# Kernel optimization log

Measured on AMD Instinct MI355X. Metric: run time of the kernel, lower is better.

Reference implementation:

```python
import jax, jax.numpy as jnp
import numpy as np

L, C, F, H, W = 4, 512, 2048, 8, 4   # layers, channels, filter, heads, window
HD = C // H                          # head_dim = 64
B, T = 4, 1024
EPS = 1e-6


def setup_inputs() -> dict:
    key = jax.random.key(0)
    ks = jax.random.split(key, 12)
    def n(k, shape, s=0.02):
        return jax.random.normal(k, shape, dtype=jnp.float32) * s
    return {
        "x": jax.random.normal(ks[0], (B, C, T), dtype=jnp.float32),
        "mask": jnp.ones((B, 1, T), dtype=jnp.float32),
        "qw": n(ks[1], (L, C, C)), "qb": jnp.zeros((L, C), jnp.float32),
        "kw": n(ks[2], (L, C, C)), "kb": jnp.zeros((L, C), jnp.float32),
        "vw": n(ks[3], (L, C, C)), "vb": jnp.zeros((L, C), jnp.float32),
        "ow": n(ks[4], (L, C, C)), "ob": jnp.zeros((L, C), jnp.float32),
        "emb_rel_k": n(ks[5], (L, 2 * W + 1, HD), 0.01),
        "emb_rel_v": n(ks[6], (L, 2 * W + 1, HD), 0.01),
        "ln1_g": jnp.ones((L, C), jnp.float32), "ln1_b": jnp.zeros((L, C), jnp.float32),
        "w1": n(ks[7], (L, F, C)), "b1": jnp.zeros((L, F), jnp.float32),
        "w2": n(ks[8], (L, C, F)), "b2": jnp.zeros((L, C), jnp.float32),
        "ln2_g": jnp.ones((L, C), jnp.float32), "ln2_b": jnp.zeros((L, C), jnp.float32),
    }


def _conv1(x, w, b):
    # 1x1 Conv1d: (B,Cin,T) x (Cout,Cin) -> (B,Cout,T)
    return jnp.einsum('oc,bct->bot', w, x) + b[None, :, None]


def _ln(x, g, b):
    # LayerNorm over channel dim of (B,C,T)
    m = jnp.mean(x, axis=1, keepdims=True)
    v = jnp.var(x, axis=1, keepdims=True)
    return (x - m) * jax.lax.rsqrt(v + EPS) * g[None, :, None] + b[None, :, None]


def reference(x, mask, qw, qb, kw, kb, vw, vb, ow, ob, emb_rel_k, emb_rel_v,
              ln1_g, ln1_b, w1, b1, w2, b2, ln2_g, ln2_b):
    Bv, Cv, Tv = x.shape
    pos = jnp.arange(Tv)
    rel = pos[None, :] - pos[:, None]           # (T,T) j - i
    outside = jnp.abs(rel) > W
    idx = jnp.clip(rel, -W, W) + W              # (T,T) in [0, 2W]
    am = mask[:, :, None, :]                    # (B,1,1,T)
    inv_scale = 1.0 / jnp.sqrt(jnp.float32(HD))
    for i in range(L):
        res = x
        q = _conv1(x, qw[i], qb[i]).reshape(Bv, H, HD, Tv).transpose(0, 1, 3, 2) * inv_scale
        k = _conv1(x, kw[i], kb[i]).reshape(Bv, H, HD, Tv).transpose(0, 1, 3, 2)
        v = _conv1(x, vw[i], vb[i]).reshape(Bv, H, HD, Tv).transpose(0, 1, 3, 2)
        rk = jnp.where(outside[:, :, None], 0.0, emb_rel_k[i][idx])  # (T,T,HD)
        rv = jnp.where(outside[:, :, None], 0.0, emb_rel_v[i][idx])
        scores = jnp.einsum('bhid,bhjd->bhij', q, k) + jnp.einsum('bhid,ijd->bhij', q, rk)
        scores = jnp.where(am == 0, -jnp.inf, scores)
        attn = jax.nn.softmax(scores, axis=-1)
        o = jnp.einsum('bhij,bhjd->bhid', attn, v) + jnp.einsum('bhij,ijd->bhid', attn, rv)
        o = o.transpose(0, 1, 3, 2).reshape(Bv, Cv, Tv)
        x = _ln(res + _conv1(o, ow[i], ob[i]), ln1_g[i], ln1_b[i])
        res = x
        h = jax.nn.relu(_conv1(x * mask, w1[i], b1[i])) * mask
        h = _conv1(h, w2[i], b2[i]) * mask
        x = _ln(res + h, ln2_g[i], ln2_b[i])
        x = x * mask
    return x
```

## Files before the change

kernel.cpp:

```cpp
#include <hip/hip_runtime.h>

#define BQ 4
#define CQ 512
#define TQ 1024
#define FQ 2048
#define LQ 4
#define HQ 8
#define MT (BQ * TQ)

typedef __attribute__((ext_vector_type(8))) short short8;
typedef __attribute__((ext_vector_type(4))) float floatx4;

#define MFMA16(a, b, c) __builtin_amdgcn_mfma_f32_16x16x32_bf16(a, b, c, 0, 0, 0)

static __device__ __forceinline__ unsigned short f2bf(float f) {
  union { float f; unsigned u; } v; v.f = f;
  unsigned r = v.u + 0x7fff + ((v.u >> 16) & 1);
  return (unsigned short)(r >> 16);
}

static __device__ __forceinline__ void async_copy16(const void* g, void* l) {
  __builtin_amdgcn_global_load_lds(
      (const __attribute__((address_space(1))) void*)g,
      (__attribute__((address_space(3))) void*)l, 16, 0, 0);
}

__global__ __launch_bounds__(256) void mfma_gemm(
    const unsigned short* __restrict__ A, const unsigned short* __restrict__ B,
    void* __restrict__ Y, const float* __restrict__ bias,
    const float* __restrict__ mask, int M, int N, int K, int lda, int ldb,
    long long kofs, long long sYb, float scale, int flags)
{
  const int tid = threadIdx.x;
  const int w = tid >> 6, lane = tid & 63;
  const int wm = w >> 1, wn = w & 1;
  const int m0 = blockIdx.y * 128, n0 = blockIdx.x * 128;
  const size_t ko = (size_t)blockIdx.z * kofs;

  __shared__ unsigned short sA[128 * 32];
  __shared__ unsigned short sB[128 * 32];

  floatx4 acc[4][4];
#pragma unroll
  for (int i = 0; i < 4; i++)
#pragma unroll
    for (int j = 0; j < 4; j++) acc[i][j] = floatx4{0.f, 0.f, 0.f, 0.f};

  const int srow = lane >> 2;
  const int skel = (lane & 3) * 8;
  const int col = lane & 15, gq = lane >> 4;

  for (int k0 = 0; k0 < K; k0 += 32) {
#pragma unroll
    for (int r = 0; r < 2; r++) {
      int c = r * 4 + w;
      async_copy16(&A[(size_t)(m0 + c * 16 + srow) * lda + ko + k0 + skel],
                   &sA[c * 512]);
      async_copy16(&B[(size_t)(n0 + c * 16 + srow) * ldb + ko + k0 + skel],
                   &sB[c * 512]);
    }
    __syncthreads();

    short8 af[4], bfr[4];
#pragma unroll
    for (int im = 0; im < 4; im++)
      af[im] = *(const short8*)&sA[(wm * 64 + im * 16 + col) * 32 + gq * 8];
#pragma unroll
    for (int in = 0; in < 4; in++)
      bfr[in] = *(const short8*)&sB[(wn * 64 + in * 16 + col) * 32 + gq * 8];
#pragma unroll
    for (int im = 0; im < 4; im++)
#pragma unroll
      for (int in = 0; in < 4; in++)
        acc[im][in] = MFMA16(af[im], bfr[in], acc[im][in]);
    __syncthreads();
  }

  const bool relu  = flags & 1;
  const bool prem  = flags & 2;
  const bool postm = flags & 4;
  const bool bf16o = flags & 16;
  const bool raw   = flags & 32;
  float* Yf = (float*)Y + (size_t)blockIdx.z * sYb;
  unsigned short* Yh = (unsigned short*)Y;

#pragma unroll
  for (int im = 0; im < 4; im++)
#pragma unroll
    for (int in = 0; in < 4; in++) {
      int nn = n0 + wn * 64 + in * 16 + col;
      float bn = raw ? 0.f : bias[nn];
#pragma unroll
      for (int reg = 0; reg < 4; reg++) {
        int mm = m0 + wm * 64 + im * 16 + gq * 4 + reg;
        float val = acc[im][in][reg];
        if (raw) {
          Yf[(size_t)mm * N + nn] = val;
        } else {
          float mv = (prem || postm) ? mask[mm] : 1.f;
          if (prem) val *= mv;
          val = (val + bn) * scale;
          if (relu) val = fmaxf(val, 0.f);
          if (postm) val *= mv;
          if (bf16o) Yh[(size_t)mm * N + nn] = f2bf(val);
          else       Yf[(size_t)mm * N + nn] = val;
        }
      }
    }
}

__global__ __launch_bounds__(256) void mfma_gemm64(
    const unsigned short* __restrict__ A, const unsigned short* __restrict__ B,
    float* __restrict__ Y, int M, int N, int K, int lda, int ldb,
    long long kofs, long long sYb)
{
  const int tid = threadIdx.x;
  const int w = tid >> 6, lane = tid & 63;
  const int wm = w >> 1, wn = w & 1;
  const int m0 = blockIdx.y * 128, n0 = blockIdx.x * 64;
  const size_t ko = (size_t)blockIdx.z * kofs;

  __shared__ unsigned short sA[128 * 32];
  __shared__ unsigned short sB[64 * 32];

  floatx4 acc[4][2];
#pragma unroll
  for (int i = 0; i < 4; i++)
#pragma unroll
    for (int j = 0; j < 2; j++) acc[i][j] = floatx4{0.f, 0.f, 0.f, 0.f};

  const int srow = lane >> 2;
  const int skel = (lane & 3) * 8;
  const int col = lane & 15, gq = lane >> 4;

  for (int k0 = 0; k0 < K; k0 += 32) {
    async_copy16(&A[(size_t)(m0 + w * 16 + srow) * lda + ko + k0 + skel],
                 &sA[w * 512]);
    async_copy16(&A[(size_t)(m0 + (w + 4) * 16 + srow) * lda + ko + k0 + skel],
                 &sA[(w + 4) * 512]);
    async_copy16(&B[(size_t)(n0 + w * 16 + srow) * ldb + ko + k0 + skel],
                 &sB[w * 512]);
    __syncthreads();

    short8 af[4], bfr[2];
#pragma unroll
    for (int im = 0; im < 4; im++)
      af[im] = *(const short8*)&sA[(wm * 64 + im * 16 + col) * 32 + gq * 8];
#pragma unroll
    for (int in = 0; in < 2; in++)
      bfr[in] = *(const short8*)&sB[(wn * 32 + in * 16 + col) * 32 + gq * 8];
#pragma unroll
    for (int im = 0; im < 4; im++)
#pragma unroll
      for (int in = 0; in < 2; in++)
        acc[im][in] = MFMA16(af[im], bfr[in], acc[im][in]);
    __syncthreads();
  }

  float* Yf = Y + (size_t)blockIdx.z * sYb;
#pragma unroll
  for (int im = 0; im < 4; im++)
#pragma unroll
    for (int in = 0; in < 2; in++) {
      int nn = n0 + wn * 32 + in * 16 + col;
#pragma unroll
      for (int reg = 0; reg < 4; reg++) {
        int mm = m0 + wm * 64 + im * 16 + gq * 4 + reg;
        Yf[(size_t)mm * N + nn] = acc[im][in][reg];
      }
    }
}

__global__ __launch_bounds__(256) void qkv_gemm(
    const unsigned short* __restrict__ A, const unsigned short* __restrict__ B,
    unsigned short* __restrict__ qo, unsigned short* __restrict__ ko2,
    unsigned short* __restrict__ vo, const float* __restrict__ qb,
    const float* __restrict__ kb, const float* __restrict__ vb)
{
  const int tid = threadIdx.x;
  const int w = tid >> 6, lane = tid & 63;
  const int wm = w >> 1, wn = w & 1;
  const int m0 = blockIdx.y * 128, n0 = blockIdx.x * 128;

  __shared__ unsigned short sA[128 * 32];
  __shared__ unsigned short sB[128 * 32];

  floatx4 acc[4][4];
#pragma unroll
  for (int i = 0; i < 4; i++)
#pragma unroll
    for (int j = 0; j < 4; j++) acc[i][j] = floatx4{0.f, 0.f, 0.f, 0.f};

  const int srow = lane >> 2;
  const int skel = (lane & 3) * 8;
  const int col = lane & 15, gq = lane >> 4;

  for (int k0 = 0; k0 < CQ; k0 += 32) {
#pragma unroll
    for (int r = 0; r < 2; r++) {
      int c = r * 4 + w;
      async_copy16(&A[(size_t)(m0 + c * 16 + srow) * CQ + k0 + skel],
                   &sA[c * 512]);
      async_copy16(&B[(size_t)(n0 + c * 16 + srow) * CQ + k0 + skel],
                   &sB[c * 512]);
    }
    __syncthreads();

    short8 af[4], bfr[4];
#pragma unroll
    for (int im = 0; im < 4; im++)
      af[im] = *(const short8*)&sA[(wm * 64 + im * 16 + col) * 32 + gq * 8];
#pragma unroll
    for (int in = 0; in < 4; in++)
      bfr[in] = *(const short8*)&sB[(wn * 64 + in * 16 + col) * 32 + gq * 8];
#pragma unroll
    for (int im = 0; im < 4; im++)
#pragma unroll
      for (int in = 0; in < 4; in++)
        acc[im][in] = MFMA16(af[im], bfr[in], acc[im][in]);
    __syncthreads();
  }

  const int seg = n0 >> 9;
  const int nbase = n0 - seg * 512;

  if (seg < 2) {
    unsigned short* Yh = (seg == 0) ? qo : ko2;
    const float* bp = (seg == 0) ? qb : kb;
    const float scale = (seg == 0) ? 0.125f : 1.f;
#pragma unroll
    for (int im = 0; im < 4; im++)
#pragma unroll
      for (int in = 0; in < 4; in++) {
        int nn = nbase + wn * 64 + in * 16 + col;
        float bn = bp[nn];
#pragma unroll
        for (int reg = 0; reg < 4; reg++) {
          int mm = m0 + wm * 64 + im * 16 + gq * 4 + reg;
          Yh[(size_t)mm * CQ + nn] = f2bf((acc[im][in][reg] + bn) * scale);
        }
      }
  } else {
#pragma unroll
    for (int im = 0; im < 4; im++)
#pragma unroll
      for (int in = 0; in < 4; in++) {
        int nn = nbase + wn * 64 + in * 16 + col;
        float bn = vb[nn];
        int mm0 = m0 + wm * 64 + im * 16 + gq * 4;
        int bz = mm0 >> 10, t = mm0 & 1023;
        ushort4 uv = {f2bf(acc[im][in][0] + bn), f2bf(acc[im][in][1] + bn),
                      f2bf(acc[im][in][2] + bn), f2bf(acc[im][in][3] + bn)};
        *(ushort4*)&vo[((size_t)bz * CQ + nn) * TQ + t] = uv;
      }
  }
}

__global__ __launch_bounds__(256) void attn_kernel(
    const unsigned short* __restrict__ qt, const unsigned short* __restrict__ kt,
    const unsigned short* __restrict__ vt, const float* __restrict__ mask,
    const float* __restrict__ rk, const float* __restrict__ rv,
    unsigned short* __restrict__ o)
{
  const int b = blockIdx.z, h = blockIdx.y;
  const int w = threadIdx.x >> 6;
  const int lane = threadIdx.x & 63;
  const int col = lane & 15, g = lane >> 4;
  const int i0 = blockIdx.x * 64 + w * 16;

  const unsigned short* qb = qt + (size_t)b * TQ * CQ + h * 64;
  const unsigned short* kb = kt + (size_t)b * TQ * CQ + h * 64;
  const unsigned short* vb = vt + ((size_t)b * CQ + h * 64) * TQ;
  unsigned short* ob = o + (size_t)b * TQ * CQ + h * 64;

  __shared__ unsigned short sK[2][64 * 64];
  __shared__ unsigned short sV[2][64 * 64];
  __shared__ unsigned short pbuf[4][16][72];
  __shared__ float rkdl[4][16][9];
  __shared__ float pband[4][16][9];
  __shared__ float smask[TQ];

  short8 qf0 = *(const short8*)&qb[(size_t)(i0 + col) * CQ + g * 8];
  short8 qf1 = *(const short8*)&qb[(size_t)(i0 + col) * CQ + 32 + g * 8];

  {
    short8 rb0 = {0, 0, 0, 0, 0, 0, 0, 0}, rb1 = rb0;
    if (col < 9) {
#pragma unroll
      for (int i = 0; i < 8; i++) {
        rb0[i] = (short)f2bf(rk[col * 64 + g * 8 + i]);
        rb1[i] = (short)f2bf(rk[col * 64 + 32 + g * 8 + i]);
      }
    }
    floatx4 rc = {0.f, 0.f, 0.f, 0.f};
    rc = MFMA16(qf0, rb0, rc);
    rc = MFMA16(qf1, rb1, rc);
    if (col < 9) {
#pragma unroll
      for (int reg = 0; reg < 4; reg++) rkdl[w][g * 4 + reg][col] = rc[reg];
    }
  }
  for (int e = lane; e < 144; e += 64) pband[w][e / 9][e % 9] = 0.f;
  {
    float4 mvv = *(const float4*)&mask[(size_t)b * TQ + threadIdx.x * 4];
    *(float4*)&smask[threadIdx.x * 4] = mvv;
  }

  const int prow = lane >> 3;
  const int pblk = (lane & 7) ^ prow;
  const int eblk0 = ((0 * 4 + g) ^ (col & 7)) * 8;
  const int eblk1 = ((1 * 4 + g) ^ (col & 7)) * 8;

#pragma unroll
  for (int q = 0; q < 2; q++) {
    int s = w * 2 + q;
    async_copy16(&kb[(size_t)(s * 8 + prow) * CQ + pblk * 8], &sK[0][s * 512]);
    async_copy16(&vb[(size_t)(s * 8 + prow) * TQ + 0 + pblk * 8], &sV[0][s * 512]);
  }

  float l_lane[4] = {0.f, 0.f, 0.f, 0.f};
  floatx4 oacc[4];
#pragma unroll
  for (int r = 0; r < 4; r++) oacc[r] = floatx4{0.f, 0.f, 0.f, 0.f};

  for (int jt = 0; jt < 16; jt++) {
    const int cur = jt & 1, nx = cur ^ 1;
    __syncthreads();
    if (jt < 15) {
      const int j0n = (jt + 1) * 64;
#pragma unroll
      for (int q = 0; q < 2; q++) {
        int s = w * 2 + q;
        async_copy16(&kb[(size_t)(j0n + s * 8 + prow) * CQ + pblk * 8],
                     &sK[nx][s * 512]);
        async_copy16(&vb[(size_t)(s * 8 + prow) * TQ + j0n + pblk * 8],
                     &sV[nx][s * 512]);
      }
    }
    const int j0 = jt * 64;

    floatx4 sc[4];
#pragma unroll
    for (int jg = 0; jg < 4; jg++) {
      const int r = (jg * 16 + col) * 64;
      short8 kf0 = *(const short8*)&sK[cur][r + eblk0];
      short8 kf1 = *(const short8*)&sK[cur][r + eblk1];
      floatx4 z = {0.f, 0.f, 0.f, 0.f};
      z = MFMA16(qf0, kf0, z);
      sc[jg] = MFMA16(qf1, kf1, z);
    }

    const bool inband = (j0 <= i0 + 19) && (j0 + 63 >= i0 - 4);

    float p[4][4];
#pragma unroll
    for (int reg = 0; reg < 4; reg++) {
      const int ig = i0 + g * 4 + reg;
#pragma unroll
      for (int jg = 0; jg < 4; jg++) {
        float s = sc[jg][reg];
        if (inband) {
          int dlt = j0 + jg * 16 + col - ig + 4;
          if (dlt >= 0 && dlt < 9) s += rkdl[w][g * 4 + reg][dlt];
        }
        float pv = (smask[j0 + jg * 16 + col] == 0.f) ? 0.f : __expf(s);
        p[reg][jg] = pv;
        l_lane[reg] += pv;
      }
    }

    if (inband) {
#pragma unroll
      for (int reg = 0; reg < 4; reg++) {
        const int row = g * 4 + reg;
#pragma unroll
        for (int jg = 0; jg < 4; jg++) {
          int dlt = j0 + jg * 16 + col - (i0 + row) + 4;
          if (dlt >= 0 && dlt < 9) pband[w][row][dlt] = p[reg][jg];
        }
      }
    }

#pragma unroll
    for (int reg = 0; reg < 4; reg++)
#pragma unroll
      for (int jg = 0; jg < 4; jg++)
        pbuf[w][g * 4 + reg][jg * 16 + col] = f2bf(p[reg][jg]);
    __builtin_amdgcn_wave_barrier();
    short8 pf0 = *(const short8*)&pbuf[w][col][g * 8];
    short8 pf1 = *(const short8*)&pbuf[w][col][32 + g * 8];

#pragma unroll
    for (int dg = 0; dg < 4; dg++) {
      const int r = (dg * 16 + col) * 64;
      short8 vf0 = *(const short8*)&sV[cur][r + eblk0];
      short8 vf1 = *(const short8*)&sV[cur][r + eblk1];
      oacc[dg] = MFMA16(pf0, vf0, oacc[dg]);
      oacc[dg] = MFMA16(pf1, vf1, oacc[dg]);
    }
    __builtin_amdgcn_wave_barrier();
  }

  float inv_l[4];
#pragma unroll
  for (int reg = 0; reg < 4; reg++) {
    float l = l_lane[reg];
#pragma unroll
    for (int off = 1; off < 16; off <<= 1) l += __shfl_xor(l, off, 64);
    inv_l[reg] = 1.f / l;
  }

#pragma unroll
  for (int dg = 0; dg < 4; dg++) {
    float rvc[4] = {0.f, 0.f, 0.f, 0.f};
#pragma unroll
    for (int dlt = 0; dlt < 9; dlt++) {
      float rvv = rv[dlt * 64 + dg * 16 + col];
#pragma unroll
      for (int reg = 0; reg < 4; reg++)
        rvc[reg] += pband[w][g * 4 + reg][dlt] * rvv;
    }
#pragma unroll
    for (int reg = 0; reg < 4; reg++) {
      float val = (oacc[dg][reg] + rvc[reg]) * inv_l[reg];
      ob[(size_t)(i0 + g * 4 + reg) * CQ + dg * 16 + col] = f2bf(val);
    }
  }
}

__global__ __launch_bounds__(256) void ln_rows(
    const float* __restrict__ res, const float* __restrict__ a1,
    const float* __restrict__ a2, const float* __restrict__ addb,
    const float* __restrict__ g, const float* __restrict__ bb,
    const float* __restrict__ mask, float* __restrict__ outf,
    unsigned short* __restrict__ outb, int mode)
{
  const int row = blockIdx.x * 4 + (threadIdx.x >> 6);
  const int lane = threadIdx.x & 63;
  const size_t base = (size_t)row * CQ + lane * 8;
  const int c0 = lane * 8;

  float mv = mask[row];
  float sadd = (mode & 1) ? mv : 1.f;

  float v[8];
#pragma unroll
  for (int i = 0; i < 8; i += 4) {
    float4 r = *(const float4*)&res[base + i];
    float4 x1 = *(const float4*)&a1[base + i];
    float4 x2 = *(const float4*)&a2[base + i];
    float4 bv = *(const float4*)&addb[c0 + i];
    v[i + 0] = r.x + sadd * (x1.x + x2.x + bv.x);
    v[i + 1] = r.y + sadd * (x1.y + x2.y + bv.y);
    v[i + 2] = r.z + sadd * (x1.z + x2.z + bv.z);
    v[i + 3] = r.w + sadd * (x1.w + x2.w + bv.w);
  }
  float sum = 0.f, ssq = 0.f;
#pragma unroll
  for (int i = 0; i < 8; i++) { sum += v[i]; ssq += v[i] * v[i]; }
#pragma unroll
  for (int off = 1; off < 64; off <<= 1) {
    sum += __shfl_xor(sum, off, 64);
    ssq += __shfl_xor(ssq, off, 64);
  }
  float mean = sum * (1.f / CQ);
  float var = ssq * (1.f / CQ) - mean * mean;
  float rstd = rsqrtf(var + 1e-6f);
  float pm = (mode & 2) ? mv : 1.f;

  float y[8];
#pragma unroll
  for (int i = 0; i < 8; i++)
    y[i] = ((v[i] - mean) * rstd * g[c0 + i] + bb[c0 + i]) * pm;
  float4 o0 = {y[0], y[1], y[2], y[3]}, o1 = {y[4], y[5], y[6], y[7]};
  *(float4*)&outf[base] = o0;
  *(float4*)&outf[base + 4] = o1;
  if (outb) {
    ushort4 u0 = {f2bf(y[0]), f2bf(y[1]), f2bf(y[2]), f2bf(y[3])};
    ushort4 u1 = {f2bf(y[4]), f2bf(y[5]), f2bf(y[6]), f2bf(y[7])};
    *(ushort4*)&outb[base] = u0;
    *(ushort4*)&outb[base + 4] = u1;
  }
}

__global__ __launch_bounds__(256) void tr_in(
    const float* __restrict__ x, float* __restrict__ xa,
    unsigned short* __restrict__ xab)
{
  __shared__ float s[32][33];
  const int b = blockIdx.z, t0 = blockIdx.x * 32, c0 = blockIdx.y * 32;
  const int tx = threadIdx.x, ty = threadIdx.y;
#pragma unroll
  for (int r = 0; r < 4; r++)
    s[ty + r * 8][tx] = x[((size_t)b * CQ + c0 + ty + r * 8) * TQ + t0 + tx];
  __syncthreads();
#pragma unroll
  for (int r = 0; r < 4; r++) {
    float v = s[tx][ty + r * 8];
    size_t idx = ((size_t)b * TQ + t0 + ty + r * 8) * CQ + c0 + tx;
    xa[idx] = v;
    xab[idx] = f2bf(v);
  }
}

__global__ __launch_bounds__(256) void tr_out(
    const float* __restrict__ y, float* __restrict__ out)
{
  __shared__ float s[32][33];
  const int b = blockIdx.z, t0 = blockIdx.x * 32, c0 = blockIdx.y * 32;
  const int tx = threadIdx.x, ty = threadIdx.y;
#pragma unroll
  for (int r = 0; r < 4; r++)
    s[ty + r * 8][tx] = y[((size_t)b * TQ + t0 + ty + r * 8) * CQ + c0 + tx];
  __syncthreads();
#pragma unroll
  for (int r = 0; r < 4; r++)
    out[((size_t)b * CQ + c0 + ty + r * 8) * TQ + t0 + tx] = s[tx][ty + r * 8];
}

__global__ __launch_bounds__(256) void wconv(
    const float* __restrict__ qw, const float* __restrict__ kw,
    const float* __restrict__ vw, const float* __restrict__ ow,
    const float* __restrict__ w1, const float* __restrict__ w2,
    unsigned short* __restrict__ dst)
{
  int idx4 = blockIdx.x * 256 + threadIdx.x;
  int i = idx4 * 4;
  const float* src;
  int off;
  if (i < 1048576) {
    int which = i >> 18;
    src = (which == 0) ? qw : (which == 1) ? kw : (which == 2) ? vw : ow;
    off = i & 262143;
  } else if (i < 2097152) {
    src = w1; off = i - 1048576;
  } else {
    src = w2; off = i - 2097152;
  }
  float4 v = *(const float4*)&src[off];
  ushort4 u = {f2bf(v.x), f2bf(v.y), f2bf(v.z), f2bf(v.w)};
  *(ushort4*)&dst[i] = u;
}

extern "C" void kernel_launch(void* const* d_in, const int* in_sizes, int n_in,
                              void* d_out, int out_size, void* d_ws, size_t ws_size,
                              hipStream_t stream) {
  const float* x    = (const float*)d_in[0];
  const float* mask = (const float*)d_in[1];
  const float* qw   = (const float*)d_in[2];
  const float* qbb  = (const float*)d_in[3];
  const float* kw   = (const float*)d_in[4];
  const float* kbb  = (const float*)d_in[5];
  const float* vw   = (const float*)d_in[6];
  const float* vbb  = (const float*)d_in[7];
  const float* ow   = (const float*)d_in[8];
  const float* obb  = (const float*)d_in[9];
  const float* rk   = (const float*)d_in[10];
  const float* rv   = (const float*)d_in[11];
  const float* g1   = (const float*)d_in[12];
  const float* be1  = (const float*)d_in[13];
  const float* w1   = (const float*)d_in[14];
  const float* b1   = (const float*)d_in[15];
  const float* w2   = (const float*)d_in[16];
  const float* b2   = (const float*)d_in[17];
  const float* g2   = (const float*)d_in[18];
  const float* be2  = (const float*)d_in[19];
  float* out = (float*)d_out;

  const size_t MB = 1 << 20;
  char* base = (char*)d_ws;
  unsigned short* wbuf  = (unsigned short*)(base);
  float*          xa    = (float*)(base + 6 * MB);
  unsigned short* xab   = (unsigned short*)(base + 14 * MB);
  unsigned short* qtb   = (unsigned short*)(base + 18 * MB);
  unsigned short* ktb   = (unsigned short*)(base + 22 * MB);
  unsigned short* vtb   = (unsigned short*)(base + 30 * MB);
  unsigned short* obufb = (unsigned short*)(base + 34 * MB);
  float*          t1    = (float*)(base + 38 * MB);
  unsigned short* hbuf  = qtb;

  const unsigned short* wo  = wbuf + 786432;
  const unsigned short* wf1 = wbuf + 1048576;
  const unsigned short* wf2 = wbuf + 2097152;
  const long long sY = (long long)MT * CQ;
  float* t1b = t1 + sY;

  dim3 b256(256);
  dim3 gtr(TQ / 32, CQ / 32, BQ);
  dim3 gln(MT / 4);

  hipLaunchKernelGGL(tr_in, gtr, dim3(32, 8), 0, stream, x, xa, xab);

  for (int i = 0; i < LQ; i++) {
    hipLaunchKernelGGL(wconv, dim3(3072), b256, 0, stream,
        qw + (size_t)i * CQ * CQ, kw + (size_t)i * CQ * CQ,
        vw + (size_t)i * CQ * CQ, ow + (size_t)i * CQ * CQ,
        w1 + (size_t)i * FQ * CQ, w2 + (size_t)i * CQ * FQ, wbuf);
    hipLaunchKernelGGL(qkv_gemm, dim3(12, 32), b256, 0, stream,
        xab, wbuf, qtb, ktb, vtb, qbb + i * CQ, kbb + i * CQ, vbb + i * CQ);
    hipLaunchKernelGGL(attn_kernel, dim3(TQ / 64, HQ, BQ), b256, 0, stream,
        qtb, ktb, vtb, mask, rk + (size_t)i * 576, rv + (size_t)i * 576, obufb);
    hipLaunchKernelGGL(mfma_gemm64, dim3(8, 32, 2), b256, 0, stream,
        obufb, wo, t1, MT, CQ, CQ / 2, CQ, CQ, (long long)(CQ / 2), sY);
    hipLaunchKernelGGL(ln_rows, gln, b256, 0, stream,
        xa, t1, t1b, obb + i * CQ, g1 + i * CQ, be1 + i * CQ, mask,
        xa, xab, 0);
    hipLaunchKernelGGL(mfma_gemm, dim3(16, 32, 1), b256, 0, stream,
        xab, wf1, (void*)hbuf, b1 + i * FQ, mask,
        MT, FQ, CQ, CQ, CQ, 0LL, 0LL, 1.f, 1 | 2 | 4 | 16);
    hipLaunchKernelGGL(mfma_gemm64, dim3(8, 32, 2), b256, 0, stream,
        hbuf, wf2, t1, MT, CQ, FQ / 2, FQ, FQ, (long long)(FQ / 2), sY);
    hipLaunchKernelGGL(ln_rows, gln, b256, 0, stream,
        xa, t1, t1b, b2 + i * CQ, g2 + i * CQ, be2 + i * CQ, mask,
        xa, xab, 3);
  }
  hipLaunchKernelGGL(tr_out, gtr, dim3(32, 8), 0, stream, xa, out);
}
```

Before: 678.2 us.

## Double GEMM K-tile to 64 with XOR-swizzled LDS and batch weight conversion

```diff
diff --git a/kernel.cpp b/kernel.cpp
--- a/kernel.cpp
+++ b/kernel.cpp
@@ -37,8 +37,8 @@
   const int m0 = blockIdx.y * 128, n0 = blockIdx.x * 128;
   const size_t ko = (size_t)blockIdx.z * kofs;
 
-  __shared__ unsigned short sA[128 * 32];
-  __shared__ unsigned short sB[128 * 32];
+  __shared__ unsigned short sA[128 * 64];
+  __shared__ unsigned short sB[128 * 64];
 
   floatx4 acc[4][4];
 #pragma unroll
@@ -46,33 +46,37 @@
 #pragma unroll
     for (int j = 0; j < 4; j++) acc[i][j] = floatx4{0.f, 0.f, 0.f, 0.f};
 
-  const int srow = lane >> 2;
-  const int skel = (lane & 3) * 8;
   const int col = lane & 15, gq = lane >> 4;
-
-  for (int k0 = 0; k0 < K; k0 += 32) {
-#pragma unroll
-    for (int r = 0; r < 2; r++) {
-      int c = r * 4 + w;
-      async_copy16(&A[(size_t)(m0 + c * 16 + srow) * lda + ko + k0 + skel],
-                   &sA[c * 512]);
-      async_copy16(&B[(size_t)(n0 + c * 16 + srow) * ldb + ko + k0 + skel],
-                   &sB[c * 512]);
+  const int xsw = col & 7;
+
+  for (int k0 = 0; k0 < K; k0 += 64) {
+#pragma unroll
+    for (int r = 0; r < 4; r++) {
+      const int cbase = w * 64 + r * 256;
+      const int c = cbase + lane;
+      const int row = c >> 3, p = c & 7;
+      const int gb = (p ^ (row & 7)) * 8;
+      async_copy16(&A[(size_t)(m0 + row) * lda + ko + k0 + gb], &sA[cbase * 8]);
+      async_copy16(&B[(size_t)(n0 + row) * ldb + ko + k0 + gb], &sB[cbase * 8]);
     }
     __syncthreads();
-
-    short8 af[4], bfr[4];
-#pragma unroll
-    for (int im = 0; im < 4; im++)
-      af[im] = *(const short8*)&sA[(wm * 64 + im * 16 + col) * 32 + gq * 8];
-#pragma unroll
-    for (int in = 0; in < 4; in++)
-      bfr[in] = *(const short8*)&sB[(wn * 64 + in * 16 + col) * 32 + gq * 8];
-#pragma unroll
-    for (int im = 0; im < 4; im++)
+#pragma unroll
+    for (int kh = 0; kh < 2; kh++) {
+      const int q = kh * 4 + gq;
+      const int so = (q ^ xsw) * 8;
+      short8 af[4], bfr[4];
+#pragma unroll
+      for (int im = 0; im < 4; im++)
+        af[im] = *(const short8*)&sA[(wm * 64 + im * 16 + col) * 64 + so];
 #pragma unroll
       for (int in = 0; in < 4; in++)
-        acc[im][in] = MFMA16(af[im], bfr[in], acc[im][in]);
+        bfr[in] = *(const short8*)&sB[(wn * 64 + in * 16 + col) * 64 + so];
+#pragma unroll
+      for (int im = 0; im < 4; im++)
+#pragma unroll
+        for (int in = 0; in < 4; in++)
+          acc[im][in] = MFMA16(af[im], bfr[in], acc[im][in]);
+    }
     __syncthreads();
   }
 
@@ -120,8 +124,8 @@
   const int m0 = blockIdx.y * 128, n0 = blockIdx.x * 64;
   const size_t ko = (size_t)blockIdx.z * kofs;
 
-  __shared__ unsigned short sA[128 * 32];
-  __shared__ unsigned short sB[64 * 32];
+  __shared__ unsigned short sA[128 * 64];
+  __shared__ unsigned short sB[64 * 64];
 
   floatx4 acc[4][2];
 #pragma unroll
@@ -129,31 +133,44 @@
 #pragma unroll
     for (int j = 0; j < 2; j++) acc[i][j] = floatx4{0.f, 0.f, 0.f, 0.f};
 
-  const int srow = lane >> 2;
-  const int skel = (lane & 3) * 8;
   const int col = lane & 15, gq = lane >> 4;
-
-  for (int k0 = 0; k0 < K; k0 += 32) {
-    async_copy16(&A[(size_t)(m0 + w * 16 + srow) * lda + ko + k0 + skel],
-                 &sA[w * 512]);
-    async_copy16(&A[(size_t)(m0 + (w + 4) * 16 + srow) * lda + ko + k0 + skel],
-                 &sA[(w + 4) * 512]);
-    async_copy16(&B[(size_t)(n0 + w * 16 + srow) * ldb + ko + k0 + skel],
-                 &sB[w * 512]);
+  const int xsw = col & 7;
+
+  for (int k0 = 0; k0 < K; k0 += 64) {
+#pragma unroll
+    for (int r = 0; r < 4; r++) {
+      const int cbase = w * 64 + r * 256;
+      const int c = cbase + lane;
+      const int row = c >> 3, p = c & 7;
+      const int gb = (p ^ (row & 7)) * 8;
+      async_copy16(&A[(size_t)(m0 + row) * lda + ko + k0 + gb], &sA[cbase * 8]);
+    }
+#pragma unroll
+    for (int r = 0; r < 2; r++) {
+      const int cbase = w * 64 + r * 256;
+      const int c = cbase + lane;
+      const int row = c >> 3, p = c & 7;
+      const int gb = (p ^ (row & 7)) * 8;
+      async_copy16(&B[(size_t)(n0 + row) * ldb + ko + k0 + gb], &sB[cbase * 8]);
+    }
     __syncthreads();
-
-    short8 af[4], bfr[2];
-#pragma unroll
-    for (int im = 0; im < 4; im++)
-      af[im] = *(const short8*)&sA[(wm * 64 + im * 16 + col) * 32 + gq * 8];
-#pragma unroll
-    for (int in = 0; in < 2; in++)
-      bfr[in] = *(const short8*)&sB[(wn * 32 + in * 16 + col) * 32 + gq * 8];
-#pragma unroll
-    for (int im = 0; im < 4; im++)
+#pragma unroll
+    for (int kh = 0; kh < 2; kh++) {
+      const int q = kh * 4 + gq;
+      const int so = (q ^ xsw) * 8;
+      short8 af[4], bfr[2];
+#pragma unroll
+      for (int im = 0; im < 4; im++)
+        af[im] = *(const short8*)&sA[(wm * 64 + im * 16 + col) * 64 + so];
 #pragma unroll
       for (int in = 0; in < 2; in++)
-        acc[im][in] = MFMA16(af[im], bfr[in], acc[im][in]);
+        bfr[in] = *(const short8*)&sB[(wn * 32 + in * 16 + col) * 64 + so];
+#pragma unroll
+      for (int im = 0; im < 4; im++)
+#pragma unroll
+        for (int in = 0; in < 2; in++)
+          acc[im][in] = MFMA16(af[im], bfr[in], acc[im][in]);
+    }
     __syncthreads();
   }
 
@@ -182,8 +199,8 @@
   const int wm = w >> 1, wn = w & 1;
   const int m0 = blockIdx.y * 128, n0 = blockIdx.x * 128;
 
-  __shared__ unsigned short sA[128 * 32];
-  __shared__ unsigned short sB[128 * 32];
+  __shared__ unsigned short sA[128 * 64];
+  __shared__ unsigned short sB[128 * 64];
 
   floatx4 acc[4][4];
 #pragma unroll
@@ -191,33 +208,37 @@
 #pragma unroll
     for (int j = 0; j < 4; j++) acc[i][j] = floatx4{0.f, 0.f, 0.f, 0.f};
 
-  const int srow = lane >> 2;
-  const int skel = (lane & 3) * 8;
   const int col = lane & 15, gq = lane >> 4;
-
-  for (int k0 = 0; k0 < CQ; k0 += 32) {
-#pragma unroll
-    for (int r = 0; r < 2; r++) {
-      int c = r * 4 + w;
-      async_copy16(&A[(size_t)(m0 + c * 16 + srow) * CQ + k0 + skel],
-                   &sA[c * 512]);
-      async_copy16(&B[(size_t)(n0 + c * 16 + srow) * CQ + k0 + skel],
-                   &sB[c * 512]);
+  const int xsw = col & 7;
+
+  for (int k0 = 0; k0 < CQ; k0 += 64) {
+#pragma unroll
+    for (int r = 0; r < 4; r++) {
+      const int cbase = w * 64 + r * 256;
+      const int c = cbase + lane;
+      const int row = c >> 3, p = c & 7;
+      const int gb = (p ^ (row & 7)) * 8;
+      async_copy16(&A[(size_t)(m0 + row) * CQ + k0 + gb], &sA[cbase * 8]);
+      async_copy16(&B[(size_t)(n0 + row) * CQ + k0 + gb], &sB[cbase * 8]);
     }
     __syncthreads();
-
-    short8 af[4], bfr[4];
-#pragma unroll
-    for (int im = 0; im < 4; im++)
-      af[im] = *(const short8*)&sA[(wm * 64 + im * 16 + col) * 32 + gq * 8];
-#pragma unroll
-    for (int in = 0; in < 4; in++)
-      bfr[in] = *(const short8*)&sB[(wn * 64 + in * 16 + col) * 32 + gq * 8];
-#pragma unroll
-    for (int im = 0; im < 4; im++)
+#pragma unroll
+    for (int kh = 0; kh < 2; kh++) {
+      const int q = kh * 4 + gq;
+      const int so = (q ^ xsw) * 8;
+      short8 af[4], bfr[4];
+#pragma unroll
+      for (int im = 0; im < 4; im++)
+        af[im] = *(const short8*)&sA[(wm * 64 + im * 16 + col) * 64 + so];
 #pragma unroll
       for (int in = 0; in < 4; in++)
-        acc[im][in] = MFMA16(af[im], bfr[in], acc[im][in]);
+        bfr[in] = *(const short8*)&sB[(wn * 64 + in * 16 + col) * 64 + so];
+#pragma unroll
+      for (int im = 0; im < 4; im++)
+#pragma unroll
+        for (int in = 0; in < 4; in++)
+          acc[im][in] = MFMA16(af[im], bfr[in], acc[im][in]);
+    }
     __syncthreads();
   }
 
@@ -518,28 +539,32 @@
     out[((size_t)b * CQ + c0 + ty + r * 8) * TQ + t0 + tx] = s[tx][ty + r * 8];
 }
 
-__global__ __launch_bounds__(256) void wconv(
+__global__ __launch_bounds__(256) void wconv_all(
     const float* __restrict__ qw, const float* __restrict__ kw,
     const float* __restrict__ vw, const float* __restrict__ ow,
     const float* __restrict__ w1, const float* __restrict__ w2,
     unsigned short* __restrict__ dst)
 {
+  const int PER_L4 = 786432;
   int idx4 = blockIdx.x * 256 + threadIdx.x;
-  int i = idx4 * 4;
+  int l = idx4 / PER_L4;
+  int e = (idx4 - l * PER_L4) * 4;
   const float* src;
-  int off;
-  if (i < 1048576) {
-    int which = i >> 18;
-    src = (which == 0) ? qw : (which == 1) ? kw : (which == 2) ? vw : ow;
-    off = i & 262143;
-  } else if (i < 2097152) {
-    src = w1; off = i - 1048576;
+  size_t off;
+  if (e < 786432) {
+    int which = e >> 18;
+    src = (which == 0) ? qw : (which == 1) ? kw : vw;
+    off = (size_t)l * 262144 + (e & 262143);
+  } else if (e < 1048576) {
+    src = ow;  off = (size_t)l * 262144 + (e - 786432);
+  } else if (e < 2097152) {
+    src = w1;  off = (size_t)l * 1048576 + (e - 1048576);
   } else {
-    src = w2; off = i - 2097152;
+    src = w2;  off = (size_t)l * 1048576 + (e - 2097152);
   }
   float4 v = *(const float4*)&src[off];
   ushort4 u = {f2bf(v.x), f2bf(v.y), f2bf(v.z), f2bf(v.w)};
-  *(ushort4*)&dst[i] = u;
+  *(ushort4*)&dst[(size_t)l * 3145728 + e] = u;
 }
 
 extern "C" void kernel_launch(void* const* d_in, const int* in_sizes, int n_in,
@@ -569,19 +594,16 @@
 
   const size_t MB = 1 << 20;
   char* base = (char*)d_ws;
-  unsigned short* wbuf  = (unsigned short*)(base);
-  float*          xa    = (float*)(base + 6 * MB);
-  unsigned short* xab   = (unsigned short*)(base + 14 * MB);
-  unsigned short* qtb   = (unsigned short*)(base + 18 * MB);
-  unsigned short* ktb   = (unsigned short*)(base + 22 * MB);
-  unsigned short* vtb   = (unsigned short*)(base + 30 * MB);
-  unsigned short* obufb = (unsigned short*)(base + 34 * MB);
-  float*          t1    = (float*)(base + 38 * MB);
+  unsigned short* wbufA = (unsigned short*)(base);
+  float*          xa    = (float*)(base + 24 * MB);
+  unsigned short* xab   = (unsigned short*)(base + 32 * MB);
+  unsigned short* qtb   = (unsigned short*)(base + 36 * MB);
+  unsigned short* ktb   = (unsigned short*)(base + 40 * MB);
+  unsigned short* vtb   = (unsigned short*)(base + 44 * MB);
+  unsigned short* obufb = (unsigned short*)(base + 48 * MB);
+  float*          t1    = (float*)(base + 52 * MB);
   unsigned short* hbuf  = qtb;
 
-  const unsigned short* wo  = wbuf + 786432;
-  const unsigned short* wf1 = wbuf + 1048576;
-  const unsigned short* wf2 = wbuf + 2097152;
   const long long sY = (long long)MT * CQ;
   float* t1b = t1 + sY;
 
@@ -590,14 +612,16 @@
   dim3 gln(MT / 4);
 
   hipLaunchKernelGGL(tr_in, gtr, dim3(32, 8), 0, stream, x, xa, xab);
+  hipLaunchKernelGGL(wconv_all, dim3(12288), b256, 0, stream,
+      qw, kw, vw, ow, w1, w2, wbufA);
 
   for (int i = 0; i < LQ; i++) {
-    hipLaunchKernelGGL(wconv, dim3(3072), b256, 0, stream,
-        qw + (size_t)i * CQ * CQ, kw + (size_t)i * CQ * CQ,
-        vw + (size_t)i * CQ * CQ, ow + (size_t)i * CQ * CQ,
-        w1 + (size_t)i * FQ * CQ, w2 + (size_t)i * CQ * FQ, wbuf);
+    const unsigned short* wl  = wbufA + (size_t)i * 3145728;
+    const unsigned short* wo  = wl + 786432;
+    const unsigned short* wf1 = wl + 1048576;
+    const unsigned short* wf2 = wl + 2097152;
     hipLaunchKernelGGL(qkv_gemm, dim3(12, 32), b256, 0, stream,
-        xab, wbuf, qtb, ktb, vtb, qbb + i * CQ, kbb + i * CQ, vbb + i * CQ);
+        xab, wl, qtb, ktb, vtb, qbb + i * CQ, kbb + i * CQ, vbb + i * CQ);
     hipLaunchKernelGGL(attn_kernel, dim3(TQ / 64, HQ, BQ), b256, 0, stream,
         qtb, ktb, vtb, mask, rk + (size_t)i * 576, rv + (size_t)i * 576, obufb);
     hipLaunchKernelGGL(mfma_gemm64, dim3(8, 32, 2), b256, 0, stream,
```

Result: faster. 634.0 us (-6.5%).
